# Optimization experiments

Hardware: AMD Instinct MI355X
Metric: run time of the kernel (lower is better)

## Reference

```python
import jax, jax.numpy as jnp
import numpy as np

NUM_HEADS = 12
ATTN_BALANCE = 0.3
ROPE_THETA = 10000.0
EPS = 1e-4


def _mp_weight(w):
    # Eval-mode MPConv weight prep: per-output-channel magnitude-preserving
    # normalize (normalize() with alpha=sqrt(1/fan_in)), then scale by gain/sqrt(fan_in).
    O = w.shape[0]
    fan = int(np.prod(w.shape[1:]))  # in_channels * 1 * 1
    wf = w.astype(jnp.float32).reshape(O, -1)
    n = jnp.linalg.norm(wf, axis=1, keepdims=True)
    wn = wf / (EPS + n / np.sqrt(fan))
    return wn / np.sqrt(fan)  # [O, fan]; 1x1 kernel -> acts as a dense matrix


def _normalize_lastdim(x):
    # normalize(y, dim=-1): denom = eps + ||x||_2 * sqrt(1/c)
    c = x.shape[-1]
    n = jnp.linalg.norm(x.astype(jnp.float32), axis=-1, keepdims=True)
    return x / (EPS + n / np.sqrt(c)).astype(x.dtype)


def _rope(q, k):
    c = q.shape[-1]
    t = q.shape[2]
    inv_freq = 1.0 / (ROPE_THETA ** (jnp.arange(0, c, 2, dtype=jnp.float32) / c))  # [c/2]
    ang = jnp.arange(t, dtype=jnp.float32)[:, None] * inv_freq                      # [t, c/2]
    cos = jnp.cos(ang)[None, None, :, None, :]
    sin = jnp.sin(ang)[None, None, :, None, :]

    def rot(x):
        x1, x2 = jnp.split(x, 2, axis=-1)
        return jnp.concatenate([x1 * cos - x2 * sin, x2 * cos + x1 * sin], axis=-1)

    return rot(q), rot(k)


def setup_inputs() -> dict:
    key = jax.random.key(0)
    k1, k2, k3 = jax.random.split(key, 3)
    B, C, H, W = 32, 768, 16, 16  # B = batch_size * n_frames = 2 * 16
    x = jax.random.normal(k1, (B, C, H, W), dtype=jnp.float32)
    w_qkv = jax.random.normal(k2, (3 * C, C, 1, 1), dtype=jnp.float32)
    w_proj = jax.random.normal(k3, (C, C, 1, 1), dtype=jnp.float32)
    return {"x": x, "w_qkv": w_qkv, "w_proj": w_proj, "batch_size": 2}


def reference(x, w_qkv, w_proj, batch_size):
    B, C, H, W = x.shape
    m = NUM_HEADS
    c = C // m
    t = B // batch_size
    i = H * W
    T = t * i

    wq = _mp_weight(w_qkv).astype(x.dtype)   # [3C, C]
    wp = _mp_weight(w_proj).astype(x.dtype)  # [C, C]

    # 1x1 conv == channel matmul
    y = jnp.einsum('bchw,oc->bohw', x, wq)
    # '(b t) (s m c) h w -> b s m t (h w) c'
    y = y.reshape(batch_size, t, 3, m, c, i).transpose(0, 2, 3, 1, 5, 4)  # [b,3,m,t,i,c]
    y = _normalize_lastdim(y)
    q, k, v = y[:, 0], y[:, 1], y[:, 2]  # each [b, m, t, i, c]
    q, k = _rope(q, k)

    q = q.reshape(batch_size, m, T, c)
    k = k.reshape(batch_size, m, T, c)
    v = v.reshape(batch_size, m, T, c)

    # frame-causal block mask: q_frame >= kv_frame (infer-mode mask of the module)
    scores = jnp.einsum('bmqc,bmkc->bmqk', q, k) / np.sqrt(c)
    frame = jnp.arange(T) // i
    mask = frame[:, None] >= frame[None, :]  # [T, T] bool, block structure over frames
    scores = jnp.where(mask, scores, -jnp.inf)
    attn = jax.nn.softmax(scores, axis=-1)
    o = jnp.einsum('bmqk,bmkc->bmqc', attn, v)

    # 'b m (t h w) c -> (b t) (c m) h w'  (channel index = c_idx * m + m_idx)
    o = o.reshape(batch_size, m, t, H, W, c).transpose(0, 2, 5, 1, 3, 4).reshape(B, C, H, W)
    o = jnp.einsum('bchw,oc->bohw', o, wp)

    tt = ATTN_BALANCE  # mp_sum(x, o, t)
    return (x + tt * (o - x)) / np.sqrt((1.0 - tt) ** 2 + tt ** 2)
```

## Files before the change

### kernel.cpp

```cpp
#include <hip/hip_runtime.h>
#include <hip/hip_bf16.h>
#include <math.h>

typedef __hip_bfloat16 bf16;
typedef __attribute__((ext_vector_type(8))) short short8;
typedef __attribute__((ext_vector_type(4))) float f32x4;

#define EPSV 0.0001f

__device__ __forceinline__ unsigned short f2bf(float f) {
    unsigned int u = __float_as_uint(f);
    u += 0x7fff + ((u >> 16) & 1);
    return (unsigned short)(u >> 16);
}
__device__ __forceinline__ unsigned int pkbf(float a, float b) {
    __hip_bfloat162 h = __float22bfloat162_rn(make_float2(a, b));
    return *(unsigned int*)&h;
}
__device__ __forceinline__ float fast_exp2(float x) {
    return __builtin_amdgcn_exp2f(x);
}

__global__ __launch_bounds__(256) void rownorm_cast_kernel(
    const float* __restrict__ w_qkv, const float* __restrict__ w_proj,
    unsigned short* __restrict__ Wqb, unsigned short* __restrict__ Wpb)
{
    const int row = blockIdx.x;
    const float* src;
    unsigned short* dst;
    if (row < 2304) { src = w_qkv + (size_t)row * 768;           dst = Wqb + (size_t)row * 768; }
    else            { src = w_proj + (size_t)(row - 2304) * 768; dst = Wpb + (size_t)(row - 2304) * 768; }

    const int tid = threadIdx.x;
    float v[3];
    float ss = 0.f;
    #pragma unroll
    for (int j = 0; j < 3; j++) {
        v[j] = src[tid + j * 256];
        ss += v[j] * v[j];
    }
    #pragma unroll
    for (int off = 32; off > 0; off >>= 1) ss += __shfl_down(ss, off, 64);
    __shared__ float wsum[4];
    if ((tid & 63) == 0) wsum[tid >> 6] = ss;
    __syncthreads();
    const float total = wsum[0] + wsum[1] + wsum[2] + wsum[3];
    const float scale = 1.0f / (EPSV * 27.712812921102035f + sqrtf(total));
    #pragma unroll
    for (int j = 0; j < 3; j++) dst[tid + j * 256] = f2bf(v[j] * scale);
}

__global__ __launch_bounds__(256) void cast_x_kernel(
    const float* __restrict__ X, unsigned short* __restrict__ XbT)
{
    const int c0 = blockIdx.x * 64;
    const int b  = blockIdx.y;
    const int pos = threadIdx.x;
    const float* src = X + ((size_t)b * 768 + c0) * 256 + pos;
    unsigned short* dst = XbT + ((size_t)b * 256 + pos) * 768 + c0;
    #pragma unroll
    for (int cc = 0; cc < 8; cc++) {
        short8 t;
        #pragma unroll
        for (int j = 0; j < 8; j++)
            t[j] = (short)f2bf(src[(size_t)(cc * 8 + j) * 256]);
        *(short8*)&dst[cc * 8] = t;
    }
}

__global__ __launch_bounds__(256, 2) void qkv_mfma_kernel(
    const unsigned short* __restrict__ Wqb,
    const unsigned short* __restrict__ XbT,
    bf16* __restrict__ Q, bf16* __restrict__ K, bf16* __restrict__ Vt)
{
    const int g = blockIdx.x;
    const int b = blockIdx.y;
    const int bs = b >> 4, fr = b & 15;
    const int qkv = g / 12, head = g % 12;
    const int m0 = g * 64;

    const int tid = threadIdx.x;
    const int w = tid >> 6, lane = tid & 63;
    const int l15 = lane & 15, quad = lane >> 4;

    __shared__ unsigned short As[64 * 72];
    __shared__ unsigned short Bs[256 * 72];

    const unsigned short* Ag = Wqb + (size_t)m0 * 768;
    const unsigned short* Bg = XbT + (size_t)b * 256 * 768;

    f32x4 acc[4][4];
    #pragma unroll
    for (int mi = 0; mi < 4; mi++)
        #pragma unroll
        for (int ni = 0; ni < 4; ni++)
            acc[mi][ni] = (f32x4){0.f, 0.f, 0.f, 0.f};

    const int arow = tid >> 2, acol = (tid & 3) * 16;
    const int brow = tid >> 3, bcol = (tid & 7) * 8;

    for (int k0 = 0; k0 < 768; k0 += 64) {
        const short8 av0 = *(const short8*)&Ag[(size_t)arow * 768 + k0 + acol];
        const short8 av1 = *(const short8*)&Ag[(size_t)arow * 768 + k0 + acol + 8];
        short8 bv[8];
        #pragma unroll
        for (int p = 0; p < 8; p++)
            bv[p] = *(const short8*)&Bg[(size_t)(32 * p + brow) * 768 + k0 + bcol];
        __syncthreads();
        *(short8*)&As[arow * 72 + acol] = av0;
        *(short8*)&As[arow * 72 + acol + 8] = av1;
        #pragma unroll
        for (int p = 0; p < 8; p++)
            *(short8*)&Bs[(32 * p + brow) * 72 + bcol] = bv[p];
        __syncthreads();

        short8 af[4][2], bfr[4][2];
        #pragma unroll
        for (int mi = 0; mi < 4; mi++)
            #pragma unroll
            for (int kk = 0; kk < 2; kk++)
                af[mi][kk] = *(const short8*)&As[(16 * mi + l15) * 72 + 32 * kk + 8 * quad];
        #pragma unroll
        for (int ni = 0; ni < 4; ni++)
            #pragma unroll
            for (int kk = 0; kk < 2; kk++)
                bfr[ni][kk] = *(const short8*)&Bs[(64 * w + 16 * ni + l15) * 72 + 32 * kk + 8 * quad];
        #pragma unroll
        for (int kk = 0; kk < 2; kk++)
            #pragma unroll
            for (int mi = 0; mi < 4; mi++)
                #pragma unroll
                for (int ni = 0; ni < 4; ni++)
                    acc[mi][ni] = __builtin_amdgcn_mfma_f32_16x16x32_bf16(af[mi][kk], bfr[ni][kk], acc[mi][ni], 0, 0, 0);
    }

    float inv[4];
    #pragma unroll
    for (int ni = 0; ni < 4; ni++) {
        float ssq = 0.f;
        #pragma unroll
        for (int mi = 0; mi < 4; mi++)
            #pragma unroll
            for (int r = 0; r < 4; r++)
                ssq = fmaf(acc[mi][ni][r], acc[mi][ni][r], ssq);
        ssq += __shfl_xor(ssq, 16, 64);
        ssq += __shfl_xor(ssq, 32, 64);
        inv[ni] = 1.0f / (EPSV + sqrtf(ssq) * 0.125f);
    }

    if (qkv == 2) {
        unsigned short* Vb = &Bs[w * 64 * 72];
        #pragma unroll
        for (int ni = 0; ni < 4; ni++)
            #pragma unroll
            for (int mi = 0; mi < 4; mi++) {
                uint2 d;
                d.x = pkbf(acc[mi][ni][0] * inv[ni], acc[mi][ni][1] * inv[ni]);
                d.y = pkbf(acc[mi][ni][2] * inv[ni], acc[mi][ni][3] * inv[ni]);
                *(uint2*)&Vb[(16 * ni + l15) * 72 + 16 * mi + 4 * quad] = d;
            }
        unsigned short* Vtu = (unsigned short*)Vt;
        const size_t cb = ((size_t)(bs * 12 + head) * 64);
        const int tok = fr * 256 + 64 * w + lane;
        #pragma unroll 8
        for (int ch = 0; ch < 64; ch++)
            Vtu[(cb + ch) * 4096 + tok] = Vb[lane * 72 + ch];
    } else {
        unsigned short* dst = (unsigned short*)((qkv == 0) ? Q : K);
        const float post = (qkv == 0) ? 0.125f : 1.0f;
        #pragma unroll
        for (int ni = 0; ni < 4; ni++) {
            const int token = fr * 256 + 64 * w + 16 * ni + l15;
            const size_t base = (((size_t)(bs * 12 + head)) * 4096 + token) * 64;
            #pragma unroll
            for (int mi = 0; mi < 2; mi++) {
                unsigned int lo[2], hi[2];
                #pragma unroll
                for (int r = 0; r < 4; r++) {
                    const int j = 16 * mi + 4 * quad + r;
                    const float n1 = acc[mi][ni][r] * inv[ni];
                    const float n2 = acc[mi + 2][ni][r] * inv[ni];
                    const float ang = (float)fr * exp2f(-(float)j * 0.41524101186092029f);
                    float sn, cs;
                    __sincosf(ang, &sn, &cs);
                    const unsigned short o1 = f2bf((n1 * cs - n2 * sn) * post);
                    const unsigned short o2 = f2bf((n2 * cs + n1 * sn) * post);
                    if (r < 2) { if (r == 0) { lo[0] = o1; hi[0] = o2; } else { lo[0] |= (unsigned int)o1 << 16; hi[0] |= (unsigned int)o2 << 16; } }
                    else       { if (r == 2) { lo[1] = o1; hi[1] = o2; } else { lo[1] |= (unsigned int)o1 << 16; hi[1] |= (unsigned int)o2 << 16; } }
                }
                *(uint2*)&dst[base + 16 * mi + 4 * quad]      = make_uint2(lo[0], lo[1]);
                *(uint2*)&dst[base + 32 + 16 * mi + 4 * quad] = make_uint2(hi[0], hi[1]);
            }
        }
    }
}

__global__ __launch_bounds__(256, 3) void attn_mfma_kernel(
    const bf16* __restrict__ Qg, const bf16* __restrict__ Kg,
    const bf16* __restrict__ Vtg, unsigned short* __restrict__ OspT)
{
    const int px = blockIdx.x;
    const int p = px >> 2, sub = px & 3;
    const int fa = p, fb = 15 - p;
    const int head = blockIdx.y, bs = blockIdx.z;
    const int tid = threadIdx.x;
    const int w = tid >> 6, lane = tid & 63;
    const int l15 = lane & 15, quad = lane >> 4;
    const size_t hb = ((size_t)(bs * 12 + head)) * 4096 * 64;

    __shared__ unsigned short Vs[64 * 72];
    __shared__ unsigned short Pw[2][64 * 72];
    __shared__ float Lred[2][4][16][4];

    const unsigned short* Qu = (const unsigned short*)Qg;
    const unsigned short* Ku = (const unsigned short*)Kg;
    const unsigned short* Vu = (const unsigned short*)Vtg;

    short8 Qfa[4][2], Qfb[4][2];
    #pragma unroll
    for (int ni = 0; ni < 4; ni++) {
        const int qra = fa * 256 + sub * 64 + 16 * ni + l15;
        const int qrb = fb * 256 + sub * 64 + 16 * ni + l15;
        #pragma unroll
        for (int kk = 0; kk < 2; kk++) {
            Qfa[ni][kk] = *(const short8*)&Qu[hb + (size_t)qra * 64 + 32 * kk + 8 * quad];
            Qfb[ni][kk] = *(const short8*)&Qu[hb + (size_t)qrb * 64 + 32 * kk + 8 * quad];
        }
    }

    f32x4 Oa[4], Ob[4];
    #pragma unroll
    for (int c = 0; c < 4; c++) {
        Oa[c] = (f32x4){0.f, 0.f, 0.f, 0.f};
        Ob[c] = (f32x4){0.f, 0.f, 0.f, 0.f};
    }
    float lSa[4] = {0.f, 0.f, 0.f, 0.f};
    float lSb[4] = {0.f, 0.f, 0.f, 0.f};
    const f32x4 zf = (f32x4){0.f, 0.f, 0.f, 0.f};
    const float L2E = 1.4426950408889634f;
    const float C = 11.541560327111707f;

    const int stage_row = tid >> 2;
    const int stage_off = (tid & 3) * 16;
    const unsigned short* Vst = Vu + hb + (size_t)stage_row * 4096 + stage_off;
    const unsigned short* Klane = Ku + hb + (size_t)(16 * w + l15) * 64 + 8 * quad;

    short8 va = *(const short8*)&Vst[0];
    short8 vb = *(const short8*)&Vst[8];

    const int nka = (fa + 1) * 256;
    const int nkb = (fb + 1) * 256;
    for (int t0 = 0; t0 < nkb; t0 += 64) {
        __syncthreads();
        const short8 kf0 = *(const short8*)&Klane[(size_t)t0 * 64];
        const short8 kf1 = *(const short8*)&Klane[(size_t)t0 * 64 + 32];
        *(short8*)&Vs[stage_row * 72 + stage_off] = va;
        *(short8*)&Vs[stage_row * 72 + stage_off + 8] = vb;
        __syncthreads();

        const int tn = (t0 + 64 < nkb) ? t0 + 64 : t0;
        va = *(const short8*)&Vst[tn];
        vb = *(const short8*)&Vst[tn + 8];

        const bool doA = (t0 < nka);

        {
            f32x4 St[4];
            #pragma unroll
            for (int ni = 0; ni < 4; ni++) {
                f32x4 s = __builtin_amdgcn_mfma_f32_16x16x32_bf16(kf0, Qfb[ni][0], zf, 0, 0, 0);
                St[ni] = __builtin_amdgcn_mfma_f32_16x16x32_bf16(kf1, Qfb[ni][1], s, 0, 0, 0);
            }
            #pragma unroll
            for (int ni = 0; ni < 4; ni++) {
                const f32x4 s = St[ni];
                const float p0 = fast_exp2(fmaf(s[0], L2E, -C));
                const float p1 = fast_exp2(fmaf(s[1], L2E, -C));
                const float p2 = fast_exp2(fmaf(s[2], L2E, -C));
                const float p3 = fast_exp2(fmaf(s[3], L2E, -C));
                lSb[ni] += (p0 + p1) + (p2 + p3);
                uint2 d;
                d.x = pkbf(p0, p1);
                d.y = pkbf(p2, p3);
                *(uint2*)&Pw[1][(16 * ni + l15) * 72 + 16 * w + 4 * quad] = d;
            }
            if (doA) {
                #pragma unroll
                for (int ni = 0; ni < 4; ni++) {
                    f32x4 s = __builtin_amdgcn_mfma_f32_16x16x32_bf16(kf0, Qfa[ni][0], zf, 0, 0, 0);
                    St[ni] = __builtin_amdgcn_mfma_f32_16x16x32_bf16(kf1, Qfa[ni][1], s, 0, 0, 0);
                }
                #pragma unroll
                for (int ni = 0; ni < 4; ni++) {
                    const f32x4 s = St[ni];
                    const float p0 = fast_exp2(fmaf(s[0], L2E, -C));
                    const float p1 = fast_exp2(fmaf(s[1], L2E, -C));
                    const float p2 = fast_exp2(fmaf(s[2], L2E, -C));
                    const float p3 = fast_exp2(fmaf(s[3], L2E, -C));
                    lSa[ni] += (p0 + p1) + (p2 + p3);
                    uint2 d;
                    d.x = pkbf(p0, p1);
                    d.y = pkbf(p2, p3);
                    *(uint2*)&Pw[0][(16 * ni + l15) * 72 + 16 * w + 4 * quad] = d;
                }
            }
        }
        __syncthreads();

        short8 Pfb[2], Pfa[2];
        #pragma unroll
        for (int ks = 0; ks < 2; ks++)
            Pfb[ks] = *(const short8*)&Pw[1][(16 * w + l15) * 72 + 32 * ks + 8 * quad];
        if (doA) {
            #pragma unroll
            for (int ks = 0; ks < 2; ks++)
                Pfa[ks] = *(const short8*)&Pw[0][(16 * w + l15) * 72 + 32 * ks + 8 * quad];
        }
        #pragma unroll
        for (int ci = 0; ci < 4; ci++) {
            const short8 vf0 = *(const short8*)&Vs[(16 * ci + l15) * 72 + 8 * quad];
            const short8 vf1 = *(const short8*)&Vs[(16 * ci + l15) * 72 + 32 + 8 * quad];
            Ob[ci] = __builtin_amdgcn_mfma_f32_16x16x32_bf16(Pfb[0], vf0, Ob[ci], 0, 0, 0);
            Ob[ci] = __builtin_amdgcn_mfma_f32_16x16x32_bf16(Pfb[1], vf1, Ob[ci], 0, 0, 0);
            if (doA) {
                Oa[ci] = __builtin_amdgcn_mfma_f32_16x16x32_bf16(Pfa[0], vf0, Oa[ci], 0, 0, 0);
                Oa[ci] = __builtin_amdgcn_mfma_f32_16x16x32_bf16(Pfa[1], vf1, Oa[ci], 0, 0, 0);
            }
        }
    }

    #pragma unroll
    for (int ni = 0; ni < 4; ni++) {
        lSa[ni] += __shfl_xor(lSa[ni], 16, 64);
        lSa[ni] += __shfl_xor(lSa[ni], 32, 64);
        lSb[ni] += __shfl_xor(lSb[ni], 16, 64);
        lSb[ni] += __shfl_xor(lSb[ni], 32, 64);
    }
    __syncthreads();
    if (quad == 0) {
        #pragma unroll
        for (int ni = 0; ni < 4; ni++) {
            Lred[0][ni][l15][w] = lSa[ni];
            Lred[1][ni][l15][w] = lSb[ni];
        }
    }
    __syncthreads();
    const f32x4 ra = *(const f32x4*)&Lred[0][w][l15][0];
    const f32x4 rb = *(const f32x4*)&Lred[1][w][l15][0];
    float la = 1.0f / ((ra[0] + ra[1]) + (ra[2] + ra[3]));
    float lb = 1.0f / ((rb[0] + rb[1]) + (rb[2] + rb[3]));

    const size_t oba = ((size_t)(bs * 16 + fa)) * 196608;
    const size_t obb = ((size_t)(bs * 16 + fb)) * 196608;
    #pragma unroll
    for (int r = 0; r < 4; r++) {
        const float ia = __shfl(la, quad * 4 + r, 64);
        const float ib = __shfl(lb, quad * 4 + r, 64);
        const int pos = sub * 64 + w * 16 + 4 * quad + r;
        #pragma unroll
        for (int ci = 0; ci < 4; ci++) {
            const int chan = (16 * ci + l15) * 12 + head;
            OspT[oba + (size_t)pos * 768 + chan] = f2bf(Oa[ci][r] * ia);
            OspT[obb + (size_t)pos * 768 + chan] = f2bf(Ob[ci][r] * ib);
        }
    }
}

__global__ __launch_bounds__(256, 2) void proj_mfma_kernel(
    const unsigned short* __restrict__ Wpb,
    const unsigned short* __restrict__ OspT,
    const float* __restrict__ X,
    float* __restrict__ Out)
{
    const int my = blockIdx.x;
    const int b  = blockIdx.y;
    const int m0 = my * 64;

    const int tid = threadIdx.x;
    const int w = tid >> 6, lane = tid & 63;
    const int l15 = lane & 15, quad = lane >> 4;

    __shared__ unsigned short As[64 * 72];
    __shared__ unsigned short Bs[256 * 72];

    const unsigned short* Ag = Wpb + (size_t)m0 * 768;
    const unsigned short* Bg = OspT + (size_t)b * 256 * 768;

    f32x4 acc[4][4];
    #pragma unroll
    for (int mi = 0; mi < 4; mi++)
        #pragma unroll
        for (int ni = 0; ni < 4; ni++)
            acc[mi][ni] = (f32x4){0.f, 0.f, 0.f, 0.f};

    const int arow = tid >> 2, acol = (tid & 3) * 16;
    const int brow = tid >> 3, bcol = (tid & 7) * 8;

    for (int k0 = 0; k0 < 768; k0 += 64) {
        const short8 av0 = *(const short8*)&Ag[(size_t)arow * 768 + k0 + acol];
        const short8 av1 = *(const short8*)&Ag[(size_t)arow * 768 + k0 + acol + 8];
        short8 bv[8];
        #pragma unroll
        for (int p = 0; p < 8; p++)
            bv[p] = *(const short8*)&Bg[(size_t)(32 * p + brow) * 768 + k0 + bcol];
        __syncthreads();
        *(short8*)&As[arow * 72 + acol] = av0;
        *(short8*)&As[arow * 72 + acol + 8] = av1;
        #pragma unroll
        for (int p = 0; p < 8; p++)
            *(short8*)&Bs[(32 * p + brow) * 72 + bcol] = bv[p];
        __syncthreads();

        short8 af[4][2], bfr[4][2];
        #pragma unroll
        for (int mi = 0; mi < 4; mi++)
            #pragma unroll
            for (int kk = 0; kk < 2; kk++)
                af[mi][kk] = *(const short8*)&As[(16 * mi + l15) * 72 + 32 * kk + 8 * quad];
        #pragma unroll
        for (int ni = 0; ni < 4; ni++)
            #pragma unroll
            for (int kk = 0; kk < 2; kk++)
                bfr[ni][kk] = *(const short8*)&Bs[(64 * w + 16 * ni + l15) * 72 + 32 * kk + 8 * quad];
        #pragma unroll
        for (int kk = 0; kk < 2; kk++)
            #pragma unroll
            for (int mi = 0; mi < 4; mi++)
                #pragma unroll
                for (int ni = 0; ni < 4; ni++)
                    acc[mi][ni] = __builtin_amdgcn_mfma_f32_16x16x32_bf16(af[mi][kk], bfr[ni][kk], acc[mi][ni], 0, 0, 0);
    }

    const float kMix = 1.3130643285972254f;
    #pragma unroll
    for (int mi = 0; mi < 4; mi++)
        #pragma unroll
        for (int r = 0; r < 4; r++) {
            const int m = m0 + 16 * mi + 4 * quad + r;
            const size_t rowb = (size_t)b * 196608 + (size_t)m * 256;
            #pragma unroll
            for (int ni = 0; ni < 4; ni++) {
                const int n = 64 * w + 16 * ni + l15;
                Out[rowb + n] = (0.7f * X[rowb + n] + 0.3f * acc[mi][ni][r]) * kMix;
            }
        }
}

extern "C" void kernel_launch(void* const* d_in, const int* in_sizes, int n_in,
                              void* d_out, int out_size, void* d_ws, size_t ws_size,
                              hipStream_t stream) {
    const float* x     = (const float*)d_in[0];
    const float* wqkv  = (const float*)d_in[1];
    const float* wproj = (const float*)d_in[2];
    float* out = (float*)d_out;

    char* ws = (char*)d_ws;
    unsigned short* Wqb  = (unsigned short*)(ws + 0);
    unsigned short* Wpb  = (unsigned short*)(ws + 3538944);
    unsigned short* XbT  = (unsigned short*)(ws + 4718592);
    unsigned short* OspT = XbT;
    bf16*  Q   = (bf16*)(ws + 17301504);
    bf16*  K   = (bf16*)(ws + 29884416);
    bf16*  Vt  = (bf16*)(ws + 42467328);

    rownorm_cast_kernel<<<3072, 256, 0, stream>>>(wqkv, wproj, Wqb, Wpb);
    cast_x_kernel<<<dim3(12, 32), 256, 0, stream>>>(x, XbT);
    qkv_mfma_kernel<<<dim3(36, 32), 256, 0, stream>>>(Wqb, XbT, Q, K, Vt);
    attn_mfma_kernel<<<dim3(32, 12, 2), 256, 0, stream>>>(Q, K, Vt, OspT);
    proj_mfma_kernel<<<dim3(12, 32), 256, 0, stream>>>(Wpb, OspT, x, out);
}
```

Before: 265.6 us.

## Halve query rows per attention block and split PV work across wave pairs

Each attention block now handles 32 query rows per frame instead of 64, which doubles the grid to 64x12x2 and raises the occupancy hint to 4 blocks per CU. In the PV stage, waves 0-1 accumulate the early frame and waves 2-3 the late frame, so each wave keeps a single O accumulator instead of two. This cuts register and LDS use and adds parallelism. The cost is that each K/V tile is now loaded by twice as many blocks, and waves 0-1 sit idle in the PV stage once the early frame's causal range is finished.

```diff
diff --git a/kernel.cpp b/kernel.cpp
--- a/kernel.cpp
+++ b/kernel.cpp
@@ -195,12 +195,12 @@
     }
 }
 
-__global__ __launch_bounds__(256, 3) void attn_mfma_kernel(
+__global__ __launch_bounds__(256, 4) void attn_mfma_kernel(
     const bf16* __restrict__ Qg, const bf16* __restrict__ Kg,
     const bf16* __restrict__ Vtg, unsigned short* __restrict__ OspT)
 {
     const int px = blockIdx.x;
-    const int p = px >> 2, sub = px & 3;
+    const int p = px >> 3, sub = px & 7;
     const int fa = p, fb = 15 - p;
     const int head = blockIdx.y, bs = blockIdx.z;
     const int tid = threadIdx.x;
@@ -209,18 +209,18 @@
     const size_t hb = ((size_t)(bs * 12 + head)) * 4096 * 64;
 
     __shared__ unsigned short Vs[64 * 72];
-    __shared__ unsigned short Pw[2][64 * 72];
-    __shared__ float Lred[2][4][16][4];
+    __shared__ unsigned short Pw[2][32 * 72];
+    __shared__ float Lred[2][2][16][4];
 
     const unsigned short* Qu = (const unsigned short*)Qg;
     const unsigned short* Ku = (const unsigned short*)Kg;
     const unsigned short* Vu = (const unsigned short*)Vtg;
 
-    short8 Qfa[4][2], Qfb[4][2];
-    #pragma unroll
-    for (int ni = 0; ni < 4; ni++) {
-        const int qra = fa * 256 + sub * 64 + 16 * ni + l15;
-        const int qrb = fb * 256 + sub * 64 + 16 * ni + l15;
+    short8 Qfa[2][2], Qfb[2][2];
+    #pragma unroll
+    for (int ni = 0; ni < 2; ni++) {
+        const int qra = fa * 256 + sub * 32 + 16 * ni + l15;
+        const int qrb = fb * 256 + sub * 32 + 16 * ni + l15;
         #pragma unroll
         for (int kk = 0; kk < 2; kk++) {
             Qfa[ni][kk] = *(const short8*)&Qu[hb + (size_t)qra * 64 + 32 * kk + 8 * quad];
@@ -228,14 +228,12 @@
         }
     }
 
-    f32x4 Oa[4], Ob[4];
-    #pragma unroll
-    for (int c = 0; c < 4; c++) {
-        Oa[c] = (f32x4){0.f, 0.f, 0.f, 0.f};
-        Ob[c] = (f32x4){0.f, 0.f, 0.f, 0.f};
-    }
-    float lSa[4] = {0.f, 0.f, 0.f, 0.f};
-    float lSb[4] = {0.f, 0.f, 0.f, 0.f};
+    const int tw = w >> 1;
+    f32x4 O[4];
+    #pragma unroll
+    for (int c = 0; c < 4; c++) O[c] = (f32x4){0.f, 0.f, 0.f, 0.f};
+    float lSa[2] = {0.f, 0.f};
+    float lSb[2] = {0.f, 0.f};
     const f32x4 zf = (f32x4){0.f, 0.f, 0.f, 0.f};
     const float L2E = 1.4426950408889634f;
     const float C = 11.541560327111707f;
@@ -265,14 +263,14 @@
         const bool doA = (t0 < nka);
 
         {
-            f32x4 St[4];
-            #pragma unroll
-            for (int ni = 0; ni < 4; ni++) {
+            f32x4 St[2];
+            #pragma unroll
+            for (int ni = 0; ni < 2; ni++) {
                 f32x4 s = __builtin_amdgcn_mfma_f32_16x16x32_bf16(kf0, Qfb[ni][0], zf, 0, 0, 0);
                 St[ni] = __builtin_amdgcn_mfma_f32_16x16x32_bf16(kf1, Qfb[ni][1], s, 0, 0, 0);
             }
             #pragma unroll
-            for (int ni = 0; ni < 4; ni++) {
+            for (int ni = 0; ni < 2; ni++) {
                 const f32x4 s = St[ni];
                 const float p0 = fast_exp2(fmaf(s[0], L2E, -C));
                 const float p1 = fast_exp2(fmaf(s[1], L2E, -C));
@@ -286,12 +284,12 @@
             }
             if (doA) {
                 #pragma unroll
-                for (int ni = 0; ni < 4; ni++) {
+                for (int ni = 0; ni < 2; ni++) {
                     f32x4 s = __builtin_amdgcn_mfma_f32_16x16x32_bf16(kf0, Qfa[ni][0], zf, 0, 0, 0);
                     St[ni] = __builtin_amdgcn_mfma_f32_16x16x32_bf16(kf1, Qfa[ni][1], s, 0, 0, 0);
                 }
                 #pragma unroll
-                for (int ni = 0; ni < 4; ni++) {
+                for (int ni = 0; ni < 2; ni++) {
                     const f32x4 s = St[ni];
                     const float p0 = fast_exp2(fmaf(s[0], L2E, -C));
                     const float p1 = fast_exp2(fmaf(s[1], L2E, -C));
@@ -307,30 +305,23 @@
         }
         __syncthreads();
 
-        short8 Pfb[2], Pfa[2];
-        #pragma unroll
-        for (int ks = 0; ks < 2; ks++)
-            Pfb[ks] = *(const short8*)&Pw[1][(16 * w + l15) * 72 + 32 * ks + 8 * quad];
-        if (doA) {
+        if (tw == 1 || doA) {
+            short8 Pf[2];
             #pragma unroll
             for (int ks = 0; ks < 2; ks++)
-                Pfa[ks] = *(const short8*)&Pw[0][(16 * w + l15) * 72 + 32 * ks + 8 * quad];
-        }
-        #pragma unroll
-        for (int ci = 0; ci < 4; ci++) {
-            const short8 vf0 = *(const short8*)&Vs[(16 * ci + l15) * 72 + 8 * quad];
-            const short8 vf1 = *(const short8*)&Vs[(16 * ci + l15) * 72 + 32 + 8 * quad];
-            Ob[ci] = __builtin_amdgcn_mfma_f32_16x16x32_bf16(Pfb[0], vf0, Ob[ci], 0, 0, 0);
-            Ob[ci] = __builtin_amdgcn_mfma_f32_16x16x32_bf16(Pfb[1], vf1, Ob[ci], 0, 0, 0);
-            if (doA) {
-                Oa[ci] = __builtin_amdgcn_mfma_f32_16x16x32_bf16(Pfa[0], vf0, Oa[ci], 0, 0, 0);
-                Oa[ci] = __builtin_amdgcn_mfma_f32_16x16x32_bf16(Pfa[1], vf1, Oa[ci], 0, 0, 0);
-            }
-        }
-    }
-
-    #pragma unroll
-    for (int ni = 0; ni < 4; ni++) {
+                Pf[ks] = *(const short8*)&Pw[tw][(16 * (w & 1) + l15) * 72 + 32 * ks + 8 * quad];
+            #pragma unroll
+            for (int ci = 0; ci < 4; ci++) {
+                const short8 vf0 = *(const short8*)&Vs[(16 * ci + l15) * 72 + 8 * quad];
+                const short8 vf1 = *(const short8*)&Vs[(16 * ci + l15) * 72 + 32 + 8 * quad];
+                O[ci] = __builtin_amdgcn_mfma_f32_16x16x32_bf16(Pf[0], vf0, O[ci], 0, 0, 0);
+                O[ci] = __builtin_amdgcn_mfma_f32_16x16x32_bf16(Pf[1], vf1, O[ci], 0, 0, 0);
+            }
+        }
+    }
+
+    #pragma unroll
+    for (int ni = 0; ni < 2; ni++) {
         lSa[ni] += __shfl_xor(lSa[ni], 16, 64);
         lSa[ni] += __shfl_xor(lSa[ni], 32, 64);
         lSb[ni] += __shfl_xor(lSb[ni], 16, 64);
@@ -339,29 +330,25 @@
     __syncthreads();
     if (quad == 0) {
         #pragma unroll
-        for (int ni = 0; ni < 4; ni++) {
+        for (int ni = 0; ni < 2; ni++) {
             Lred[0][ni][l15][w] = lSa[ni];
             Lred[1][ni][l15][w] = lSb[ni];
         }
     }
     __syncthreads();
-    const f32x4 ra = *(const f32x4*)&Lred[0][w][l15][0];
-    const f32x4 rb = *(const f32x4*)&Lred[1][w][l15][0];
-    float la = 1.0f / ((ra[0] + ra[1]) + (ra[2] + ra[3]));
-    float lb = 1.0f / ((rb[0] + rb[1]) + (rb[2] + rb[3]));
-
-    const size_t oba = ((size_t)(bs * 16 + fa)) * 196608;
-    const size_t obb = ((size_t)(bs * 16 + fb)) * 196608;
+    const f32x4 rr = *(const f32x4*)&Lred[tw][w & 1][l15][0];
+    float linv = 1.0f / ((rr[0] + rr[1]) + (rr[2] + rr[3]));
+
+    const int frame = tw ? fb : fa;
+    const size_t ob = ((size_t)(bs * 16 + frame)) * 196608;
     #pragma unroll
     for (int r = 0; r < 4; r++) {
-        const float ia = __shfl(la, quad * 4 + r, 64);
-        const float ib = __shfl(lb, quad * 4 + r, 64);
-        const int pos = sub * 64 + w * 16 + 4 * quad + r;
+        const float iv = __shfl(linv, quad * 4 + r, 64);
+        const int pos = sub * 32 + 16 * (w & 1) + 4 * quad + r;
         #pragma unroll
         for (int ci = 0; ci < 4; ci++) {
             const int chan = (16 * ci + l15) * 12 + head;
-            OspT[oba + (size_t)pos * 768 + chan] = f2bf(Oa[ci][r] * ia);
-            OspT[obb + (size_t)pos * 768 + chan] = f2bf(Ob[ci][r] * ib);
+            OspT[ob + (size_t)pos * 768 + chan] = f2bf(O[ci][r] * iv);
         }
     }
 }
@@ -466,6 +453,6 @@
     rownorm_cast_kernel<<<3072, 256, 0, stream>>>(wqkv, wproj, Wqb, Wpb);
     cast_x_kernel<<<dim3(12, 32), 256, 0, stream>>>(x, XbT);
     qkv_mfma_kernel<<<dim3(36, 32), 256, 0, stream>>>(Wqb, XbT, Q, K, Vt);
-    attn_mfma_kernel<<<dim3(32, 12, 2), 256, 0, stream>>>(Q, K, Vt, OspT);
+    attn_mfma_kernel<<<dim3(64, 12, 2), 256, 0, stream>>>(Q, K, Vt, OspT);
     proj_mfma_kernel<<<dim3(12, 32), 256, 0, stream>>>(Wpb, OspT, x, out);
 }
```

New measurement: 310.3 us. 16.8% more time.
